# Kernel optimization log

Hardware: AMD Instinct MI355X
Metric: run time of the kernel (lower is better)

The kernel has to match this reference:

```python
import jax, jax.numpy as jnp
import numpy as np

B, LQ, LK, D, H = 4, 2048, 2048, 1024, 16
HD = D // H  # head dim = 64


def setup_inputs() -> dict:
    key = jax.random.key(0)
    ks = jax.random.split(key, 8)
    s = 1.0 / np.sqrt(D)
    return {
        "zt": jax.random.normal(ks[0], (B, LQ, D), jnp.float32),
        "ic": jax.random.normal(ks[1], (B, LK, D), jnp.float32),
        "Wq": jax.random.normal(ks[2], (D, D), jnp.float32) * s,
        "bq": jax.random.normal(ks[3], (D,), jnp.float32) * 0.01,
        "Wk": jax.random.normal(ks[4], (D, D), jnp.float32) * s,
        "bk": jax.random.normal(ks[5], (D,), jnp.float32) * 0.01,
        "Wv": jax.random.normal(ks[6], (D, D), jnp.float32) * s,
        "bv": jax.random.normal(ks[7], (D,), jnp.float32) * 0.01,
    }


def reference(zt, ic, Wq, bq, Wk, bk, Wv, bv):
    # Linear projections (torch Linear: x @ W.T + b); weights here stored as [out, in]
    q = zt @ Wq.T + bq            # [B, LQ, D]
    k = ic @ Wk.T + bk            # [B, LK, D]
    v = ic @ Wv.T + bv            # [B, LK, D]
    # split heads -> [B, H, L, HD]
    q = q.reshape(B, LQ, H, HD).transpose(0, 2, 1, 3)
    k = k.reshape(B, LK, H, HD).transpose(0, 2, 1, 3)
    v = v.reshape(B, LK, H, HD).transpose(0, 2, 1, 3)
    scale = 1.0 / jnp.sqrt(jnp.asarray(HD, q.dtype))
    scores = jnp.einsum('bhqd,bhkd->bhqk', q, k) * scale  # [B, H, LQ, LK]
    attn = jax.nn.softmax(scores, axis=-1)
    out = jnp.einsum('bhqk,bhkd->bhqd', attn, v)          # [B, H, LQ, HD]
    return out.transpose(0, 2, 1, 3).reshape(B, LQ, D)
```

## Files before the change

### kernel.cpp

```cpp
#include <hip/hip_runtime.h>
#include <hip/hip_bf16.h>
#include <cstdint>

#define B_  4
#define LQ_ 2048
#define LK_ 2048
#define D_  1024
#define H_  16
#define HD_ 64

typedef __attribute__((ext_vector_type(8))) short bf16x8;
typedef __attribute__((ext_vector_type(4))) float f32x4;

#if defined(__has_builtin)
#if __has_builtin(__builtin_amdgcn_exp2f)
#define EXP2F(x) __builtin_amdgcn_exp2f(x)
#else
#define EXP2F(x) exp2f(x)
#endif
#else
#define EXP2F(x) exp2f(x)
#endif

__device__ __forceinline__ unsigned short f2b(float f) {
    union { float f; unsigned u; } v; v.f = f;
    unsigned u = v.u;
    unsigned r = (u + 0x7fffu + ((u >> 16) & 1u)) >> 16;
    return (unsigned short)r;
}

__device__ __forceinline__ void gl_lds16(const unsigned short* g, unsigned short* l) {
    __builtin_amdgcn_global_load_lds(
        (const __attribute__((address_space(1))) unsigned int*)(g),
        (__attribute__((address_space(3))) unsigned int*)(l),
        16, 0, 0);
}

#define PHASE_BARRIER() do { \
    __builtin_amdgcn_sched_barrier(0); \
    __builtin_amdgcn_s_barrier(); \
    __builtin_amdgcn_sched_barrier(0); } while (0)

#define WAITVM(N) do { \
    asm volatile("s_waitcnt vmcnt(" #N ")" ::: "memory"); \
    __builtin_amdgcn_sched_barrier(0); } while (0)

__global__ void cvt_all(const float* __restrict__ a0, unsigned short* __restrict__ d0,
                        const float* __restrict__ a1, unsigned short* __restrict__ d1,
                        const float* __restrict__ w0, unsigned short* __restrict__ e0, float s0,
                        const float* __restrict__ w1, unsigned short* __restrict__ e1,
                        const float* __restrict__ w2, unsigned short* __restrict__ e2,
                        int nact, int nw) {
    const float* in; unsigned short* out; float s = 1.0f; int n;
    switch (blockIdx.y) {
        case 0: in = a0; out = d0; n = nact; break;
        case 1: in = a1; out = d1; n = nact; break;
        case 2: in = w0; out = e0; n = nw; s = s0; break;
        case 3: in = w1; out = e1; n = nw; break;
        default: in = w2; out = e2; n = nw; break;
    }
    int i = (blockIdx.x * blockDim.x + threadIdx.x) * 8;
    int stride = gridDim.x * blockDim.x * 8;
    for (; i < n; i += stride) {
        float4 x = *(const float4*)(in + i);
        float4 y = *(const float4*)(in + i + 4);
        bf16x8 v;
        v[0] = (short)f2b(x.x * s); v[1] = (short)f2b(x.y * s);
        v[2] = (short)f2b(x.z * s); v[3] = (short)f2b(x.w * s);
        v[4] = (short)f2b(y.x * s); v[5] = (short)f2b(y.y * s);
        v[6] = (short)f2b(y.z * s); v[7] = (short)f2b(y.w * s);
        *(bf16x8*)(out + i) = v;
    }
}

__global__ __launch_bounds__(512, 2) void qkv_gemm(
    const unsigned short* __restrict__ Xq,
    const unsigned short* __restrict__ Xkv,
    const unsigned short* __restrict__ Wqb, const unsigned short* __restrict__ Wkb,
    const unsigned short* __restrict__ Wvb,
    const float* __restrict__ bq, const float* __restrict__ bk,
    const float* __restrict__ bv, float qscale,
    unsigned short* __restrict__ Qb, unsigned short* __restrict__ Kb,
    unsigned short* __restrict__ Vtb)
{
    __shared__ unsigned short AS[4][16 * 512];
    __shared__ unsigned short BS[4][8 * 512];

    const int proj = blockIdx.y >> 3;
    const int nt0  = blockIdx.y & 7;
    const unsigned short* X = (proj == 0) ? Xq : Xkv;
    const unsigned short* W = (proj == 0) ? Wqb : (proj == 1 ? Wkb : Wvb);
    const float* bias       = (proj == 0) ? bq  : (proj == 1 ? bk  : bv);
    const float bscale      = (proj == 0) ? qscale : 1.0f;

    const int tid  = threadIdx.x;
    const int lane = tid & 63;
    const int w    = tid >> 6;
    const int wm   = w & 1, wn = w >> 1;
    const int m0   = blockIdx.x * 256;
    const int n0   = nt0 * 128;
    const int l15  = lane & 15, quad = lane >> 4;

    f32x4 acc[8][2] = {};

    const unsigned short* gA0 = X + (size_t)(m0 + (w * 2) * 16 + l15) * 1024 + quad * 8;
    const unsigned short* gA1 = gA0 + 16 * 1024;
    const unsigned short* gB0 = W + (size_t)(n0 + w * 16 + l15) * 1024 + quad * 8;

#define STAGE(slot, koff) do { \
    gl_lds16(gA0 + (koff), &AS[slot][(w * 2) * 512 + lane * 8]); \
    gl_lds16(gA1 + (koff), &AS[slot][(w * 2 + 1) * 512 + lane * 8]); \
    gl_lds16(gB0 + (koff), &BS[slot][w * 512 + lane * 8]); } while (0)

    const int aoff = (wm * 8) * 512 + lane * 8;
    const int boff = (wn * 2) * 512 + lane * 8;

    STAGE(0, 0);
    STAGE(1, 32);
    STAGE(2, 64);

#define QPHASE(slot, WN, do_stage, sslot, skoff) do { \
    WAITVM(WN); \
    PHASE_BARRIER(); \
    bf16x8 af[8], b0, b1; \
    _Pragma("unroll") \
    for (int i = 0; i < 8; ++i) \
        af[i] = *(const bf16x8*)(&AS[slot][aoff + i * 512]); \
    b0 = *(const bf16x8*)(&BS[slot][boff]); \
    b1 = *(const bf16x8*)(&BS[slot][boff + 512]); \
    __builtin_amdgcn_s_setprio(1); \
    _Pragma("unroll") \
    for (int i = 0; i < 8; ++i) { \
        acc[i][0] = __builtin_amdgcn_mfma_f32_16x16x32_bf16(af[i], b0, acc[i][0], 0, 0, 0); \
        acc[i][1] = __builtin_amdgcn_mfma_f32_16x16x32_bf16(af[i], b1, acc[i][1], 0, 0, 0); \
    } \
    __builtin_amdgcn_s_setprio(0); \
    if (do_stage) STAGE(sslot, skoff); } while (0)

    #pragma unroll 2
    for (int t = 0; t < 16; ++t) {
        const int s0 = (2 * t) & 3;
        const int s1 = (2 * t + 1) & 3;
        const int sa = (2 * t + 3) & 3;
        const int sb = (2 * t + 4) & 3;

        if (t < 15) {
            QPHASE(s0, 6, 1, sa, (2 * t + 3) * 32);
        } else {
            QPHASE(s0, 3, 0, sa, 0);
        }
        if (t < 15) {
            QPHASE(s1, 6, (t <= 13), sb, (2 * t + 4) * 32);
        } else {
            QPHASE(s1, 0, 0, sb, 0);
        }
    }

#undef QPHASE
#undef STAGE

    float bvv[2];
    #pragma unroll
    for (int j = 0; j < 2; ++j)
        bvv[j] = bias[n0 + wn * 32 + j * 16 + l15] * bscale;

    if (proj == 2) {
        #pragma unroll
        for (int i = 0; i < 8; ++i) {
            int row = m0 + wm * 128 + i * 16 + quad * 4;
            int bb  = row >> 11;
            int tt  = row & 2047;
            #pragma unroll
            for (int j = 0; j < 2; ++j) {
                int col = n0 + wn * 32 + j * 16 + l15;
                unsigned s0v = f2b(acc[i][j][0] + bvv[j]);
                unsigned s1v = f2b(acc[i][j][1] + bvv[j]);
                unsigned s2v = f2b(acc[i][j][2] + bvv[j]);
                unsigned s3v = f2b(acc[i][j][3] + bvv[j]);
                uint2 pk;
                pk.x = s0v | (s1v << 16);
                pk.y = s2v | (s3v << 16);
                *(uint2*)(Vtb + ((size_t)(bb * 1024 + col)) * 2048 + tt) = pk;
            }
        }
    } else {
        unsigned short* Y = (proj == 0) ? Qb : Kb;
        #pragma unroll
        for (int i = 0; i < 8; ++i) {
            #pragma unroll
            for (int r = 0; r < 4; ++r) {
                int row = m0 + wm * 128 + i * 16 + quad * 4 + r;
                unsigned short* yp = Y + (size_t)row * 1024 + n0 + wn * 32;
                #pragma unroll
                for (int j = 0; j < 2; ++j)
                    yp[j * 16 + l15] = f2b(acc[i][j][r] + bvv[j]);
            }
        }
    }
}

__global__ __launch_bounds__(256, 2) void attn_kernel(
    const unsigned short* __restrict__ Q,
    const unsigned short* __restrict__ Kp,
    const unsigned short* __restrict__ Vt,
    float* __restrict__ Out)
{
    __shared__ unsigned short Ks[2][16 * 512];
    __shared__ unsigned short Vs[16 * 512];
    __shared__ unsigned short Ps[4][4096];

    const int tid  = threadIdx.x;
    const int lane = tid & 63;
    const int w    = tid >> 6;
    const int l15  = lane & 15, quad = lane >> 4;

    const int bid = blockIdx.x + (blockIdx.y << 3) + (blockIdx.z << 7);
    const int glo = bid & 7;
    const int jx  = bid >> 3;
    const int qt  = jx & 7;
    const int g   = glo + ((jx >> 3) << 3);
    const int h   = g & 15;
    const int b   = g >> 4;

    bf16x8 qf[4][2];
    #pragma unroll
    for (int half = 0; half < 4; ++half) {
        const unsigned short* qptr =
            Q + (size_t)(b * LQ_ + qt * 256 + w * 64 + half * 16 + l15) * 1024 + h * 64;
        qf[half][0] = *(const bf16x8*)(qptr + quad * 8);
        qf[half][1] = *(const bf16x8*)(qptr + 32 + quad * 8);
    }

    bf16x8 ones;
    #pragma unroll
    for (int j = 0; j < 8; ++j) ones[j] = (short)0x3F80;

    f32x4 oacc[4][4] = {};
    f32x4 lacc[4]    = {};

    const unsigned short* Kbase = Kp + (size_t)b * LK_ * 1024 + h * 64;
    const unsigned short* Vbase = Vt + (size_t)(b * 16 + h) * 64 * 2048;

    const unsigned short* gK[4];
    unsigned short* lK[4];
    const unsigned short* gV[4];
    unsigned short* lV[4];
    #pragma unroll
    for (int j = 0; j < 4; ++j) {
        int kt = w + (j >> 1) * 4, dblk = j & 1;
        gK[j] = Kbase + (size_t)(kt * 16 + l15) * 1024 + dblk * 32 + quad * 8;
        lK[j] = &Ks[0][(kt * 2 + dblk) * 512 + lane * 8];
        gV[j] = Vbase + (size_t)(w * 16 + l15) * 2048 + j * 32 + quad * 8;
        lV[j] = &Vs[(w * 4 + j) * 512 + lane * 8];
    }

    const int pws = (quad >> 1) * 128 + l15 * 8 + (quad & 1) * 4;
    unsigned short* PwB = &Ps[w][pws];
    const unsigned short* PrB = &Ps[w][lane * 8];
    const unsigned short* KfrB = &Ks[0][lane * 8];
    const unsigned short* Vfr = &Vs[lane * 8];

    #pragma unroll
    for (int j = 0; j < 4; ++j) gl_lds16(gK[j], lK[j]);

    for (int t = 0; t < 16; ++t) {
        const int cur = t & 1;
        const int k0 = t * 128;

        #pragma unroll
        for (int j = 0; j < 4; ++j) gl_lds16(gV[j] + k0, lV[j]);
        if (t < 15) {
            const int stoff = (cur ^ 1) * 8192;
            #pragma unroll
            for (int j = 0; j < 4; ++j)
                gl_lds16(gK[j] + (size_t)(t + 1) * (128 * 1024), lK[j] + stoff);
        }
        if (t == 0) {
            WAITVM(8);
            PHASE_BARRIER();
        }
        const unsigned short* Kfr = KfrB + cur * 8192;

        #pragma unroll
        for (int cc = 0; cc < 2; ++cc) {
            f32x4 st[4][4] = {};
            __builtin_amdgcn_s_setprio(1);
            #pragma unroll
            for (int ti = 0; ti < 4; ++ti)
                #pragma unroll
                for (int dblk = 0; dblk < 2; ++dblk) {
                    bf16x8 kf = *(const bf16x8*)(Kfr + ((cc * 4 + ti) * 2 + dblk) * 512);
                    #pragma unroll
                    for (int half = 0; half < 4; ++half)
                        st[half][ti] = __builtin_amdgcn_mfma_f32_16x16x32_bf16(
                            kf, qf[half][dblk], st[half][ti], 0, 0, 0);
                }
            __builtin_amdgcn_s_setprio(0);

            #pragma unroll
            for (int half = 0; half < 4; ++half) {
                unsigned short* pw = PwB + half * 1024;
                #pragma unroll
                for (int ti = 0; ti < 4; ++ti) {
                    unsigned u0 = __float_as_uint(EXP2F(st[half][ti][0])) + 0x8000u;
                    unsigned u1 = __float_as_uint(EXP2F(st[half][ti][1])) + 0x8000u;
                    unsigned u2 = __float_as_uint(EXP2F(st[half][ti][2])) + 0x8000u;
                    unsigned u3 = __float_as_uint(EXP2F(st[half][ti][3])) + 0x8000u;
                    uint2 pk;
                    pk.x = __builtin_amdgcn_perm(u1, u0, 0x07060302);
                    pk.y = __builtin_amdgcn_perm(u3, u2, 0x07060302);
                    *(uint2*)(pw + ti * 256) = pk;
                }
            }

            if (cc == 0) {
                if (t < 15) { WAITVM(4); } else { WAITVM(0); }
                PHASE_BARRIER();
            }

            #pragma unroll
            for (int hbl = 0; hbl < 2; ++hbl) {
                bf16x8 pf[4];
                __builtin_amdgcn_s_setprio(1);
                #pragma unroll
                for (int half = 0; half < 4; ++half) {
                    pf[half] = *(const bf16x8*)(PrB + half * 1024 + hbl * 512);
                    lacc[half] = __builtin_amdgcn_mfma_f32_16x16x32_bf16(
                        pf[half], ones, lacc[half], 0, 0, 0);
                }
                int hb = cc * 2 + hbl;
                #pragma unroll
                for (int nt = 0; nt < 4; ++nt) {
                    bf16x8 vf = *(const bf16x8*)(Vfr + (nt * 4 + hb) * 512);
                    #pragma unroll
                    for (int half = 0; half < 4; ++half)
                        oacc[half][nt] = __builtin_amdgcn_mfma_f32_16x16x32_bf16(
                            pf[half], vf, oacc[half][nt], 0, 0, 0);
                }
                __builtin_amdgcn_s_setprio(0);
            }
        }

        if (t < 15) {
            WAITVM(0);
            PHASE_BARRIER();
        }
    }

    #pragma unroll
    for (int half = 0; half < 4; ++half) {
        float il[4];
        #pragma unroll
        for (int r = 0; r < 4; ++r) il[r] = 1.0f / lacc[half][r];
        #pragma unroll
        for (int nt = 0; nt < 4; ++nt) {
            #pragma unroll
            for (int r = 0; r < 4; ++r) {
                size_t orow = (size_t)(b * LQ_ + qt * 256 + w * 64 + half * 16 + quad * 4 + r);
                Out[orow * 1024 + h * 64 + nt * 16 + l15] = oacc[half][nt][r] * il[r];
            }
        }
    }
}

extern "C" void kernel_launch(void* const* d_in, const int* in_sizes, int n_in,
                              void* d_out, int out_size, void* d_ws, size_t ws_size,
                              hipStream_t stream) {
    const float* zt = (const float*)d_in[0];
    const float* ic = (const float*)d_in[1];
    const float* Wq = (const float*)d_in[2];
    const float* bq = (const float*)d_in[3];
    const float* Wk = (const float*)d_in[4];
    const float* bk = (const float*)d_in[5];
    const float* Wv = (const float*)d_in[6];
    const float* bv = (const float*)d_in[7];
    float* out = (float*)d_out;

    const size_t M8 = (size_t)8192 * 1024;
    const size_t M1 = (size_t)1024 * 1024;
    unsigned short* Qb  = (unsigned short*)d_ws;
    unsigned short* Kb  = Qb  + M8;
    unsigned short* Vtb = Kb  + M8;
    unsigned short* Xz  = Vtb + M8;
    unsigned short* Xi  = Xz  + M8;
    unsigned short* Wqb = Xi  + M8;
    unsigned short* Wkb = Wqb + M1;
    unsigned short* Wvb = Wkb + M1;

    const float qscale = 0.125f * 1.44269504088896f;

    dim3 gcv(4096, 5);
    cvt_all<<<gcv, 256, 0, stream>>>(zt, Xz, ic, Xi,
                                     Wq, Wqb, qscale, Wk, Wkb, Wv, Wvb,
                                     (int)M8, (int)M1);

    dim3 gproj(32, 24);
    qkv_gemm<<<gproj, 512, 0, stream>>>(Xz, Xi, Wqb, Wkb, Wvb,
                                        bq, bk, bv, qscale, Qb, Kb, Vtb);

    dim3 gattn(8, 16, 4);
    attn_kernel<<<gattn, 256, 0, stream>>>(Qb, Kb, Vtb, out);
}
```

Baseline: 273.7 us.

## Restructure QKV GEMM pipeline to 3-stage buffers with K=64 per barrier

The QKV projection GEMM previously used a 4-slot LDS ring with a K step of 32 and one barrier per step. It now uses a 3-slot ring where each slot holds K=64 (two halves), so there is one barrier and one wait per 64-wide K step, halving synchronisation count. The prefetch distance in bytes stays similar, but LDS use rises from 96KB to 144KB per block, which likely limits the launch bound of 2 blocks per CU. That could reduce occupancy.

```diff
diff --git a/kernel.cpp b/kernel.cpp
--- a/kernel.cpp
+++ b/kernel.cpp
@@ -83,8 +83,8 @@
     unsigned short* __restrict__ Qb, unsigned short* __restrict__ Kb,
     unsigned short* __restrict__ Vtb)
 {
-    __shared__ unsigned short AS[4][16 * 512];
-    __shared__ unsigned short BS[4][8 * 512];
+    __shared__ unsigned short AS[3][16384];
+    __shared__ unsigned short BS[3][8192];
 
     const int proj = blockIdx.y >> 3;
     const int nt0  = blockIdx.y & 7;
@@ -108,55 +108,46 @@
     const unsigned short* gB0 = W + (size_t)(n0 + w * 16 + l15) * 1024 + quad * 8;
 
 #define STAGE(slot, koff) do { \
-    gl_lds16(gA0 + (koff), &AS[slot][(w * 2) * 512 + lane * 8]); \
-    gl_lds16(gA1 + (koff), &AS[slot][(w * 2 + 1) * 512 + lane * 8]); \
-    gl_lds16(gB0 + (koff), &BS[slot][w * 512 + lane * 8]); } while (0)
+    gl_lds16(gA0 + (koff),      &AS[slot][(w * 2) * 512 + lane * 8]); \
+    gl_lds16(gA1 + (koff),      &AS[slot][(w * 2 + 1) * 512 + lane * 8]); \
+    gl_lds16(gA0 + (koff) + 32, &AS[slot][8192 + (w * 2) * 512 + lane * 8]); \
+    gl_lds16(gA1 + (koff) + 32, &AS[slot][8192 + (w * 2 + 1) * 512 + lane * 8]); \
+    gl_lds16(gB0 + (koff),      &BS[slot][w * 512 + lane * 8]); \
+    gl_lds16(gB0 + (koff) + 32, &BS[slot][4096 + w * 512 + lane * 8]); } while (0)
 
     const int aoff = (wm * 8) * 512 + lane * 8;
     const int boff = (wn * 2) * 512 + lane * 8;
 
     STAGE(0, 0);
-    STAGE(1, 32);
-    STAGE(2, 64);
-
-#define QPHASE(slot, WN, do_stage, sslot, skoff) do { \
-    WAITVM(WN); \
-    PHASE_BARRIER(); \
-    bf16x8 af[8], b0, b1; \
-    _Pragma("unroll") \
-    for (int i = 0; i < 8; ++i) \
-        af[i] = *(const bf16x8*)(&AS[slot][aoff + i * 512]); \
-    b0 = *(const bf16x8*)(&BS[slot][boff]); \
-    b1 = *(const bf16x8*)(&BS[slot][boff + 512]); \
-    __builtin_amdgcn_s_setprio(1); \
-    _Pragma("unroll") \
-    for (int i = 0; i < 8; ++i) { \
-        acc[i][0] = __builtin_amdgcn_mfma_f32_16x16x32_bf16(af[i], b0, acc[i][0], 0, 0, 0); \
-        acc[i][1] = __builtin_amdgcn_mfma_f32_16x16x32_bf16(af[i], b1, acc[i][1], 0, 0, 0); \
-    } \
-    __builtin_amdgcn_s_setprio(0); \
-    if (do_stage) STAGE(sslot, skoff); } while (0)
-
-    #pragma unroll 2
-    for (int t = 0; t < 16; ++t) {
-        const int s0 = (2 * t) & 3;
-        const int s1 = (2 * t + 1) & 3;
-        const int sa = (2 * t + 3) & 3;
-        const int sb = (2 * t + 4) & 3;
-
-        if (t < 15) {
-            QPHASE(s0, 6, 1, sa, (2 * t + 3) * 32);
-        } else {
-            QPHASE(s0, 3, 0, sa, 0);
-        }
-        if (t < 15) {
-            QPHASE(s1, 6, (t <= 13), sb, (2 * t + 4) * 32);
-        } else {
-            QPHASE(s1, 0, 0, sb, 0);
-        }
-    }
-
-#undef QPHASE
+    STAGE(1, 64);
+
+    #pragma unroll
+    for (int p = 0; p < 16; ++p) {
+        const int sp = p % 3;
+
+        if (p < 15) { WAITVM(6); } else { WAITVM(0); }
+        PHASE_BARRIER();
+
+        #pragma unroll
+        for (int hh = 0; hh < 2; ++hh) {
+            bf16x8 af[8], b0, b1;
+            #pragma unroll
+            for (int i = 0; i < 8; ++i)
+                af[i] = *(const bf16x8*)(&AS[sp][hh * 8192 + aoff + i * 512]);
+            b0 = *(const bf16x8*)(&BS[sp][hh * 4096 + boff]);
+            b1 = *(const bf16x8*)(&BS[sp][hh * 4096 + boff + 512]);
+            __builtin_amdgcn_s_setprio(1);
+            #pragma unroll
+            for (int i = 0; i < 8; ++i) {
+                acc[i][0] = __builtin_amdgcn_mfma_f32_16x16x32_bf16(af[i], b0, acc[i][0], 0, 0, 0);
+                acc[i][1] = __builtin_amdgcn_mfma_f32_16x16x32_bf16(af[i], b1, acc[i][1], 0, 0, 0);
+            }
+            __builtin_amdgcn_s_setprio(0);
+        }
+
+        if (p <= 13) STAGE((p + 2) % 3, (p + 2) * 64);
+    }
+
 #undef STAGE
 
     float bvv[2];
```

Measured after the change: 272.8 us. Within noise of the previous version (-0.3%).
